# Performance work log

Measured on AMD Instinct MI355X. Metric: run time of the kernel, lower is better.

Reference implementation:

```python
import jax, jax.numpy as jnp
import numpy as np

B, S, D = 8, 1024, 1024
N_HEAD, N_ACTIVE, D_ATTN = 16, 4, 128

def setup_inputs() -> dict:
    key = jax.random.key(0)
    ks = jax.random.split(key, 8)
    sc = 0.02
    return {
        "x": jax.random.normal(ks[0], (B, S, D), jnp.float32),
        "Wq": jax.random.normal(ks[1], (N_HEAD, D, D_ATTN), jnp.float32) * sc,
        "bq": jnp.zeros((N_HEAD, D_ATTN), jnp.float32),
        "Wk": jax.random.normal(ks[2], (N_HEAD, D, D_ATTN), jnp.float32) * sc,
        "bk": jnp.zeros((N_HEAD, D_ATTN), jnp.float32),
        "Wv": jax.random.normal(ks[3], (N_HEAD, D, D_ATTN), jnp.float32) * sc,
        "bv": jnp.zeros((N_HEAD, D_ATTN), jnp.float32),
        "Wr": jax.random.normal(ks[4], (D, N_HEAD), jnp.float32) * sc,
        "br": jnp.zeros((N_HEAD,), jnp.float32),
        "Wo": jax.random.normal(ks[5], (N_ACTIVE * D_ATTN, D), jnp.float32) * sc,
        "bo": jnp.zeros((D,), jnp.float32),
    }

def reference(x, Wq, bq, Wk, bk, Wv, bv, Wr, br, Wo, bo):
    # ---- routing: mean-pool router logits over seq, softmax over heads ----
    logits = jnp.einsum('bsd,dh->bsh', x, Wr) + br          # [B,S,H]
    dist = jax.nn.softmax(logits.mean(axis=1), axis=-1)     # [B,H]
    vals, idx = jax.lax.top_k(dist, N_ACTIVE)               # [B,A]
    # zeros + scatter of top-k probs, then softmax over ALL heads (as in source)
    sparse = jnp.zeros_like(dist).at[jnp.arange(B)[:, None], idx].set(vals)
    gates_full = jax.nn.softmax(sparse, axis=-1)            # [B,H]
    gates = jnp.take_along_axis(gates_full, idx, axis=-1)   # [B,A]
    # ---- gather active-head projection weights per batch ----
    Wq_a, Wk_a, Wv_a = Wq[idx], Wk[idx], Wv[idx]            # [B,A,D,Dk]
    bq_a, bk_a, bv_a = bq[idx], bk[idx], bv[idx]            # [B,A,Dk]
    Q = jnp.einsum('bsd,badk->bask', x, Wq_a) + bq_a[:, :, None, :]
    K = jnp.einsum('bsd,badk->bask', x, Wk_a) + bk_a[:, :, None, :]
    V = jnp.einsum('bsd,badk->bask', x, Wv_a) + bv_a[:, :, None, :]
    scale = 1.0 / jnp.sqrt(jnp.asarray(D_ATTN, x.dtype))
    scores = jax.nn.softmax(jnp.einsum('bask,batk->bast', Q, K) * scale, axis=-1)
    heads = jnp.einsum('bast,batk->bask', scores, V)        # [B,A,S,Dk]
    heads = heads * gates[:, :, None, None]                 # gate each head
    # concat active heads -> [B,S,A*Dk], output projection
    cat = heads.transpose(0, 2, 1, 3).reshape(B, S, N_ACTIVE * D_ATTN)
    return jnp.einsum('bsf,fd->bsd', cat, Wo) + bo
```

## Files before the change

### kernel.cpp

```cpp
#include <hip/hip_runtime.h>
#include <math.h>

#define NB 8
#define SQ 1024
#define DM 1024
#define NH 16
#define NA 4
#define DKH 128

#define WS_XPART 0
#define WS_IDX   524288
#define WS_GATES 524416
#define WS_XB    524800
#define WS_WQT   (WS_XB  + 16777216)
#define WS_WKT   (WS_WQT + 4194304)
#define WS_WVT   (WS_WKT + 4194304)
#define WS_WOT   (WS_WVT + 4194304)
#define WS_Q     (WS_WOT + 1048576)
#define WS_K     (WS_Q  + 8388608)
#define WS_VT    (WS_K  + 8388608)
#define WS_CAT   (WS_VT + 8388608)

typedef __attribute__((ext_vector_type(8))) short short8;
typedef __attribute__((ext_vector_type(4))) short short4v;
typedef __attribute__((ext_vector_type(4))) float f32x4;

#define MFMA16(a, b, c) __builtin_amdgcn_mfma_f32_16x16x32_bf16(a, b, c, 0, 0, 0)
#define GLL16(g, l) __builtin_amdgcn_global_load_lds( \
    (const __attribute__((address_space(1))) void*)(g), \
    (__attribute__((address_space(3))) void*)(l), 16, 0, 0)

__device__ __forceinline__ short f2bf(float f) {
  unsigned u = __float_as_uint(f);
  u += 0x7FFF + ((u >> 16) & 1);
  return (short)(u >> 16);
}

__global__ __launch_bounds__(256) void k_prep(const float* __restrict__ x,
                                              short* __restrict__ xb,
                                              float* __restrict__ xpart) {
  int b = blockIdx.x, ch = blockIdx.y;
  const float* xp = x + ((size_t)b*SQ + (size_t)ch*64)*DM;
  short* xbp = xb + ((size_t)b*SQ + (size_t)ch*64)*DM;
  int t = threadIdx.x;
  float a0 = 0.f, a1 = 0.f, a2 = 0.f, a3 = 0.f;
  #pragma unroll 4
  for (int r = 0; r < 64; r++) {
    float4 v = *(const float4*)&xp[(size_t)r*DM + t*4];
    short4v s4;
    s4[0] = f2bf(v.x); s4[1] = f2bf(v.y); s4[2] = f2bf(v.z); s4[3] = f2bf(v.w);
    *(short4v*)&xbp[(size_t)r*DM + t*4] = s4;
    a0 += v.x; a1 += v.y; a2 += v.z; a3 += v.w;
  }
  float4 o = {a0, a1, a2, a3};
  *(float4*)&xpart[((size_t)b*16 + ch)*DM + t*4] = o;
}

__global__ __launch_bounds__(256) void k_tc(const float* __restrict__ in,
                                            short* __restrict__ outb, int R, int C) {
  __shared__ float t[32][33];
  int bz = blockIdx.z;
  in   += (size_t)bz * R * C;
  outb += (size_t)bz * R * C;
  int r0 = blockIdx.x * 32, c0 = blockIdx.y * 32;
  int tx = threadIdx.x, ty = threadIdx.y;
  #pragma unroll
  for (int i = 0; i < 4; i++)
    t[ty + 8*i][tx] = in[(size_t)(r0 + ty + 8*i) * C + c0 + tx];
  __syncthreads();
  #pragma unroll
  for (int i = 0; i < 4; i++)
    outb[(size_t)(c0 + ty + 8*i) * R + r0 + tx] = f2bf(t[tx][ty + 8*i]);
}

__global__ __launch_bounds__(256) void k_tcqkv(
    const float* __restrict__ Wq, const float* __restrict__ Wk,
    const float* __restrict__ Wv, short* __restrict__ Wqt,
    short* __restrict__ Wkt, short* __restrict__ Wvt) {
  __shared__ float t[32][33];
  int z = blockIdx.z;
  int m = z >> 4, hh = z & 15;
  const float* in = (m == 0 ? Wq : m == 1 ? Wk : Wv) + (size_t)hh * DM * DKH;
  short* outb = (m == 0 ? Wqt : m == 1 ? Wkt : Wvt) + (size_t)hh * DM * DKH;
  int r0 = blockIdx.x * 32, c0 = blockIdx.y * 32;
  int tx = threadIdx.x, ty = threadIdx.y;
  #pragma unroll
  for (int i = 0; i < 4; i++)
    t[ty + 8*i][tx] = in[(size_t)(r0 + ty + 8*i) * DKH + c0 + tx];
  __syncthreads();
  #pragma unroll
  for (int i = 0; i < 4; i++)
    outb[(size_t)(c0 + ty + 8*i) * DM + r0 + tx] = f2bf(t[tx][ty + 8*i]);
}

__global__ __launch_bounds__(256) void k_router(const float* __restrict__ xpart,
                                                const float* __restrict__ Wr,
                                                const float* __restrict__ br,
                                                int* __restrict__ idxout,
                                                float* __restrict__ gatesout) {
  __shared__ float xm[DM];
  __shared__ float red[16][17];
  __shared__ float logits[NH];
  int b = blockIdx.x;
  int t = threadIdx.x;
  #pragma unroll
  for (int i = 0; i < 4; i++) {
    int d = t + 256*i;
    float s = 0.f;
    for (int c = 0; c < 16; c++) s += xpart[((size_t)b*16 + c)*DM + d];
    xm[d] = s * (1.0f/(float)SQ);
  }
  __syncthreads();
  {
    int h = t & 15, c16 = t >> 4;
    float p = 0.f;
    #pragma unroll 8
    for (int j = 0; j < 64; j++) {
      int d = c16*64 + j;
      p += xm[d] * Wr[(size_t)d*NH + h];
    }
    red[c16][h] = p;
  }
  __syncthreads();
  if (t < NH) {
    float lg = br[t];
    #pragma unroll
    for (int c = 0; c < 16; c++) lg += red[c][t];
    logits[t] = lg;
  }
  __syncthreads();
  if (t == 0) {
    float mx = logits[0];
    for (int h = 1; h < NH; h++) mx = fmaxf(mx, logits[h]);
    float e[NH], sum = 0.f;
    for (int h = 0; h < NH; h++) { e[h] = expf(logits[h]-mx); sum += e[h]; }
    float dist[NH];
    for (int h = 0; h < NH; h++) dist[h] = e[h]/sum;
    int idx[NA]; float vals[NA]; bool used[NH];
    for (int h = 0; h < NH; h++) used[h] = false;
    for (int a = 0; a < NA; a++) {
      int best = -1; float bv = -1.f;
      for (int h = 0; h < NH; h++)
        if (!used[h] && dist[h] > bv) { bv = dist[h]; best = h; }
      used[best] = true; idx[a] = best; vals[a] = bv;
    }
    float sp[NH];
    for (int h = 0; h < NH; h++) sp[h] = 0.f;
    for (int a = 0; a < NA; a++) sp[idx[a]] = vals[a];
    float m2 = sp[0];
    for (int h = 1; h < NH; h++) m2 = fmaxf(m2, sp[h]);
    float e2[NH], s2 = 0.f;
    for (int h = 0; h < NH; h++) { e2[h] = expf(sp[h]-m2); s2 += e2[h]; }
    for (int a = 0; a < NA; a++) {
      idxout[b*NA + a]   = idx[a];
      gatesout[b*NA + a] = e2[idx[a]] / s2;
    }
  }
}

__global__ __launch_bounds__(256) void k_qkv(
    const short* __restrict__ xb, const short* __restrict__ Wqt,
    const short* __restrict__ Wkt, const short* __restrict__ Wvt,
    const float* __restrict__ bq, const float* __restrict__ bk,
    const float* __restrict__ bv, const int* __restrict__ idxb,
    short* __restrict__ Qo, short* __restrict__ Ko, short* __restrict__ Vto) {
  __shared__ __align__(16) short As[2][128*64];
  __shared__ __align__(16) short Bs[2][128*64];
  int mt = blockIdx.x, which = blockIdx.y, z = blockIdx.z;
  int b = z >> 2;
  int h = idxb[z];
  const short* Wt; const float* bias;
  if (which == 0)      { Wt = Wqt; bias = bq; }
  else if (which == 1) { Wt = Wkt; bias = bk; }
  else                 { Wt = Wvt; bias = bv; }
  Wt += (size_t)h * (DKH * DM);
  bias += h * DKH;
  const short* Ag = xb + (size_t)b*SQ*DM + (size_t)mt*128*DM;
  int tid = threadIdx.x, lane = tid & 63, wid = tid >> 6;
  int wm = wid & 1, wn = wid >> 1;
  int l15 = lane & 15, quad = lane >> 4, l7 = lane & 7, lby8 = lane >> 3;
  int srow = lby8;
  int scol = ((l7 ^ lby8) * 8);
  f32x4 acc[4][4];
  #pragma unroll
  for (int i = 0; i < 4; i++)
    #pragma unroll
    for (int j = 0; j < 4; j++) acc[i][j] = (f32x4){0.f,0.f,0.f,0.f};
  #pragma unroll
  for (int i = 0; i < 4; i++) {
    int ci = wid*4 + i;
    GLL16(Ag + (size_t)(ci*8 + srow)*DM + scol, &As[0][ci*512]);
    GLL16(Wt + (size_t)(ci*8 + srow)*DM + scol, &Bs[0][ci*512]);
  }
  for (int kt = 0; kt < 16; kt++) {
    int cur = kt & 1;
    asm volatile("s_waitcnt vmcnt(0)" ::: "memory");
    __syncthreads();
    if (kt + 1 < 16) {
      #pragma unroll
      for (int i = 0; i < 4; i++) {
        int ci = wid*4 + i;
        GLL16(Ag + (size_t)(ci*8 + srow)*DM + (kt+1)*64 + scol, &As[cur^1][ci*512]);
        GLL16(Wt + (size_t)(ci*8 + srow)*DM + (kt+1)*64 + scol, &Bs[cur^1][ci*512]);
      }
    }
    #pragma unroll
    for (int ks = 0; ks < 2; ks++) {
      int kc = ks*4 + quad;
      short8 a[4], bf[4];
      #pragma unroll
      for (int mi = 0; mi < 4; mi++)
        a[mi] = *(const short8*)&As[cur][(wm*64 + mi*16 + l15)*64 + ((kc ^ l7)*8)];
      #pragma unroll
      for (int ni = 0; ni < 4; ni++)
        bf[ni] = *(const short8*)&Bs[cur][(wn*64 + ni*16 + l15)*64 + ((kc ^ l7)*8)];
      #pragma unroll
      for (int mi = 0; mi < 4; mi++)
        #pragma unroll
        for (int ni = 0; ni < 4; ni++)
          acc[mi][ni] = MFMA16(a[mi], bf[ni], acc[mi][ni]);
    }
  }
  if (which < 2) {
    short* outp = (which == 0 ? Qo : Ko) + (size_t)z*SQ*DKH;
    #pragma unroll
    for (int mi = 0; mi < 4; mi++)
      #pragma unroll
      for (int ni = 0; ni < 4; ni++) {
        int col = wn*64 + ni*16 + l15;
        float bcol = bias[col];
        #pragma unroll
        for (int r = 0; r < 4; r++) {
          int row = mt*128 + wm*64 + mi*16 + quad*4 + r;
          outp[(size_t)row*DKH + col] = f2bf(acc[mi][ni][r] + bcol);
        }
      }
  } else {
    short* outp = Vto + (size_t)z*DKH*SQ;
    #pragma unroll
    for (int mi = 0; mi < 4; mi++)
      #pragma unroll
      for (int ni = 0; ni < 4; ni++) {
        int col = wn*64 + ni*16 + l15;
        float bcol = bias[col];
        int row0 = mt*128 + wm*64 + mi*16 + quad*4;
        short4v v;
        #pragma unroll
        for (int r = 0; r < 4; r++) v[r] = f2bf(acc[mi][ni][r] + bcol);
        *(short4v*)&outp[(size_t)col*SQ + row0] = v;
      }
  }
}

__global__ __launch_bounds__(256) void k_attn(
    const short* __restrict__ Qg, const short* __restrict__ Kg,
    const short* __restrict__ Vtg, const float* __restrict__ gates,
    short* __restrict__ cat) {
  __shared__ __align__(16) short Ks[2][64*128];
  __shared__ __align__(16) short Vts[2][128*64];
  __shared__ __align__(16) short Ps[4*16*72];
  int qt = blockIdx.x, z = blockIdx.y, b = z >> 2, hs = z & 3;
  int tid = threadIdx.x, lane = tid & 63, wid = tid >> 6;
  int l15 = lane & 15, quad = lane >> 4, l7 = lane & 7, lby8 = lane >> 3;
  const short* Qp = Qg + ((size_t)z*SQ + (size_t)qt*64)*DKH;
  const short* Kp = Kg + (size_t)z*SQ*DKH;
  const short* Vp = Vtg + (size_t)z*DKH*SQ;
  short8 qa[4];
  #pragma unroll
  for (int ks = 0; ks < 4; ks++)
    qa[ks] = *(const short8*)&Qp[(size_t)(wid*16 + l15)*DKH + (ks*4 + quad)*8];
  #pragma unroll
  for (int i = 0; i < 4; i++) {
    int ci = wid*4 + i;
    int r = ci*4 + quad;
    int sc = ((l15 ^ (r & 15)) * 8);
    GLL16(Kp + (size_t)r*DKH + sc, &Ks[0][ci*512]);
    int rv = ci*8 + lby8;
    int scv = ((l7 ^ lby8) * 8);
    GLL16(Vp + (size_t)rv*SQ + scv, &Vts[0][ci*512]);
  }
  f32x4 O[8];
  #pragma unroll
  for (int dn = 0; dn < 8; dn++) O[dn] = (f32x4){0.f,0.f,0.f,0.f};
  float lsum[4] = {0.f, 0.f, 0.f, 0.f};
  const float scale = 0.08838834764831845f;
  for (int t = 0; t < 16; t++) {
    int cur = t & 1;
    asm volatile("s_waitcnt vmcnt(0)" ::: "memory");
    __syncthreads();
    if (t + 1 < 16) {
      #pragma unroll
      for (int i = 0; i < 4; i++) {
        int ci = wid*4 + i;
        int r = ci*4 + quad;
        int sc = ((l15 ^ (r & 15)) * 8);
        GLL16(Kp + (size_t)((t+1)*64 + r)*DKH + sc, &Ks[cur^1][ci*512]);
        int rv = ci*8 + lby8;
        int scv = ((l7 ^ lby8) * 8);
        GLL16(Vp + (size_t)rv*SQ + (t+1)*64 + scv, &Vts[cur^1][ci*512]);
      }
    }
    f32x4 s[4];
    #pragma unroll
    for (int nj = 0; nj < 4; nj++) s[nj] = (f32x4){0.f,0.f,0.f,0.f};
    #pragma unroll
    for (int ks = 0; ks < 4; ks++) {
      int kc = ks*4 + quad;
      #pragma unroll
      for (int nj = 0; nj < 4; nj++) {
        short8 bk8 = *(const short8*)&Ks[cur][(nj*16 + l15)*128 + ((kc ^ l15)*8)];
        s[nj] = MFMA16(qa[ks], bk8, s[nj]);
      }
    }
    #pragma unroll
    for (int r = 0; r < 4; r++) {
      float p0 = __expf(s[0][r]*scale);
      float p1 = __expf(s[1][r]*scale);
      float p2 = __expf(s[2][r]*scale);
      float p3 = __expf(s[3][r]*scale);
      lsum[r] += p0 + p1 + p2 + p3;
      int pbase = wid*1152 + (quad*4 + r)*72;
      Ps[pbase +  0 + l15] = f2bf(p0);
      Ps[pbase + 16 + l15] = f2bf(p1);
      Ps[pbase + 32 + l15] = f2bf(p2);
      Ps[pbase + 48 + l15] = f2bf(p3);
    }
    asm volatile("s_waitcnt lgkmcnt(0)" ::: "memory");
    #pragma unroll
    for (int ks2 = 0; ks2 < 2; ks2++) {
      int kc = ks2*4 + quad;
      short8 pa = *(const short8*)&Ps[wid*1152 + l15*72 + kc*8];
      #pragma unroll
      for (int dn = 0; dn < 8; dn++) {
        short8 bv8 = *(const short8*)&Vts[cur][(dn*16 + l15)*64 + ((kc ^ l7)*8)];
        O[dn] = MFMA16(pa, bv8, O[dn]);
      }
    }
  }
  float gate = gates[z];
  #pragma unroll
  for (int r = 0; r < 4; r++) {
    float rs = lsum[r];
    rs += __shfl_xor(rs, 1); rs += __shfl_xor(rs, 2);
    rs += __shfl_xor(rs, 4); rs += __shfl_xor(rs, 8);
    float sc2 = gate / rs;
    int row = qt*64 + wid*16 + quad*4 + r;
    short* cp = cat + ((size_t)(b*SQ + row))*(NA*DKH) + hs*DKH;
    #pragma unroll
    for (int dn = 0; dn < 8; dn++)
      cp[dn*16 + l15] = f2bf(O[dn][r] * sc2);
  }
}

__global__ __launch_bounds__(256) void k_out(
    const short* __restrict__ catb, const short* __restrict__ Wot,
    const float* __restrict__ bo, float* __restrict__ out) {
  __shared__ __align__(16) short As[2][128*64];
  __shared__ __align__(16) short Bs[2][128*64];
  int mt = blockIdx.x, nt = blockIdx.y;
  const short* Ag = catb + (size_t)mt*128*(NA*DKH);
  const short* Bg = Wot + (size_t)nt*128*(NA*DKH);
  int tid = threadIdx.x, lane = tid & 63, wid = tid >> 6;
  int wm = wid & 1, wn = wid >> 1;
  int l15 = lane & 15, quad = lane >> 4, l7 = lane & 7, lby8 = lane >> 3;
  int srow = lby8;
  int scol = ((l7 ^ lby8) * 8);
  f32x4 acc[4][4];
  #pragma unroll
  for (int i = 0; i < 4; i++)
    #pragma unroll
    for (int j = 0; j < 4; j++) acc[i][j] = (f32x4){0.f,0.f,0.f,0.f};
  #pragma unroll
  for (int i = 0; i < 4; i++) {
    int ci = wid*4 + i;
    GLL16(Ag + (size_t)(ci*8 + srow)*(NA*DKH) + scol, &As[0][ci*512]);
    GLL16(Bg + (size_t)(ci*8 + srow)*(NA*DKH) + scol, &Bs[0][ci*512]);
  }
  for (int kt = 0; kt < 8; kt++) {
    int cur = kt & 1;
    asm volatile("s_waitcnt vmcnt(0)" ::: "memory");
    __syncthreads();
    if (kt + 1 < 8) {
      #pragma unroll
      for (int i = 0; i < 4; i++) {
        int ci = wid*4 + i;
        GLL16(Ag + (size_t)(ci*8 + srow)*(NA*DKH) + (kt+1)*64 + scol, &As[cur^1][ci*512]);
        GLL16(Bg + (size_t)(ci*8 + srow)*(NA*DKH) + (kt+1)*64 + scol, &Bs[cur^1][ci*512]);
      }
    }
    #pragma unroll
    for (int ks = 0; ks < 2; ks++) {
      int kc = ks*4 + quad;
      short8 a[4], bf[4];
      #pragma unroll
      for (int mi = 0; mi < 4; mi++)
        a[mi] = *(const short8*)&As[cur][(wm*64 + mi*16 + l15)*64 + ((kc ^ l7)*8)];
      #pragma unroll
      for (int ni = 0; ni < 4; ni++)
        bf[ni] = *(const short8*)&Bs[cur][(wn*64 + ni*16 + l15)*64 + ((kc ^ l7)*8)];
      #pragma unroll
      for (int mi = 0; mi < 4; mi++)
        #pragma unroll
        for (int ni = 0; ni < 4; ni++)
          acc[mi][ni] = MFMA16(a[mi], bf[ni], acc[mi][ni]);
    }
  }
  #pragma unroll
  for (int mi = 0; mi < 4; mi++)
    #pragma unroll
    for (int ni = 0; ni < 4; ni++) {
      int col = nt*128 + wn*64 + ni*16 + l15;
      float bcol = bo[col];
      #pragma unroll
      for (int r = 0; r < 4; r++) {
        int row = mt*128 + wm*64 + mi*16 + quad*4 + r;
        out[(size_t)row*DM + col] = acc[mi][ni][r] + bcol;
      }
    }
}

extern "C" void kernel_launch(void* const* d_in, const int* in_sizes, int n_in,
                              void* d_out, int out_size, void* d_ws, size_t ws_size,
                              hipStream_t stream) {
  const float* x  = (const float*)d_in[0];
  const float* Wq = (const float*)d_in[1];
  const float* bq = (const float*)d_in[2];
  const float* Wk = (const float*)d_in[3];
  const float* bk = (const float*)d_in[4];
  const float* Wv = (const float*)d_in[5];
  const float* bv = (const float*)d_in[6];
  const float* Wr = (const float*)d_in[7];
  const float* br = (const float*)d_in[8];
  const float* Wo = (const float*)d_in[9];
  const float* bo = (const float*)d_in[10];
  char* ws = (char*)d_ws;
  float* xpart = (float*)(ws + WS_XPART);
  int*   idxb  = (int*)(ws + WS_IDX);
  float* gat   = (float*)(ws + WS_GATES);
  short* xb    = (short*)(ws + WS_XB);
  short* Wqt   = (short*)(ws + WS_WQT);
  short* Wkt   = (short*)(ws + WS_WKT);
  short* Wvt   = (short*)(ws + WS_WVT);
  short* Wot   = (short*)(ws + WS_WOT);
  short* Qb    = (short*)(ws + WS_Q);
  short* Kb    = (short*)(ws + WS_K);
  short* Vtb   = (short*)(ws + WS_VT);
  short* catb  = (short*)(ws + WS_CAT);
  float* out   = (float*)d_out;

  k_prep<<<dim3(NB,16), 256, 0, stream>>>(x, xb, xpart);
  k_router<<<NB, 256, 0, stream>>>(xpart, Wr, br, idxb, gat);
  k_tcqkv<<<dim3(32,4,48), dim3(32,8), 0, stream>>>(Wq, Wk, Wv, Wqt, Wkt, Wvt);
  k_tc<<<dim3(16,32,1), dim3(32,8), 0, stream>>>(Wo, Wot, NA*DKH, DM);
  k_qkv<<<dim3(8,3,NB*NA), 256, 0, stream>>>(xb, Wqt, Wkt, Wvt, bq, bk, bv, idxb, Qb, Kb, Vtb);
  k_attn<<<dim3(16,NB*NA), 256, 0, stream>>>(Qb, Kb, Vtb, gat, catb);
  k_out<<<dim3(64,8), 256, 0, stream>>>(catb, Wot, bo, out);
}
```

Baseline: 237.5 us.

## Fuse weight transposes, flatten grids with XCD-aware block mapping, single-buffer QKV GEMM

Merges the Wq/Wk/Wv and Wo transpose kernels into one launch, which saves a kernel launch. The QKV, attention and output kernels now use 1D grids whose block-index mapping spreads work across the MI355X chiplets (XCDs), so blocks that share inputs land in the same L2. The QKV GEMM drops LDS double buffering and loads each tile synchronously between two barriers. That halves LDS use and should raise occupancy, but global-load latency is no longer overlapped with MFMA work.

Result: faster. 227.6 us (-4.1%).

```diff
diff --git a/kernel.cpp b/kernel.cpp
--- a/kernel.cpp
+++ b/kernel.cpp
@@ -56,13 +56,10 @@
   *(float4*)&xpart[((size_t)b*16 + ch)*DM + t*4] = o;
 }
 
-__global__ __launch_bounds__(256) void k_tc(const float* __restrict__ in,
-                                            short* __restrict__ outb, int R, int C) {
-  __shared__ float t[32][33];
-  int bz = blockIdx.z;
-  in   += (size_t)bz * R * C;
-  outb += (size_t)bz * R * C;
-  int r0 = blockIdx.x * 32, c0 = blockIdx.y * 32;
+__device__ __forceinline__ void tc_tile(const float* __restrict__ in,
+                                        short* __restrict__ outb,
+                                        int R, int C, int r0, int c0,
+                                        float (*t)[33]) {
   int tx = threadIdx.x, ty = threadIdx.y;
   #pragma unroll
   for (int i = 0; i < 4; i++)
@@ -73,24 +70,28 @@
     outb[(size_t)(c0 + ty + 8*i) * R + r0 + tx] = f2bf(t[tx][ty + 8*i]);
 }
 
-__global__ __launch_bounds__(256) void k_tcqkv(
+__global__ __launch_bounds__(256) void k_tw(
     const float* __restrict__ Wq, const float* __restrict__ Wk,
-    const float* __restrict__ Wv, short* __restrict__ Wqt,
-    short* __restrict__ Wkt, short* __restrict__ Wvt) {
+    const float* __restrict__ Wv, const float* __restrict__ Wo,
+    short* __restrict__ Wqt, short* __restrict__ Wkt,
+    short* __restrict__ Wvt, short* __restrict__ Wot) {
   __shared__ float t[32][33];
-  int z = blockIdx.z;
-  int m = z >> 4, hh = z & 15;
-  const float* in = (m == 0 ? Wq : m == 1 ? Wk : Wv) + (size_t)hh * DM * DKH;
-  short* outb = (m == 0 ? Wqt : m == 1 ? Wkt : Wvt) + (size_t)hh * DM * DKH;
-  int r0 = blockIdx.x * 32, c0 = blockIdx.y * 32;
-  int tx = threadIdx.x, ty = threadIdx.y;
-  #pragma unroll
-  for (int i = 0; i < 4; i++)
-    t[ty + 8*i][tx] = in[(size_t)(r0 + ty + 8*i) * DKH + c0 + tx];
-  __syncthreads();
-  #pragma unroll
-  for (int i = 0; i < 4; i++)
-    outb[(size_t)(c0 + ty + 8*i) * DM + r0 + tx] = f2bf(t[tx][ty + 8*i]);
+  int blk = blockIdx.x;
+  if (blk < 6144) {
+    int zz = blk >> 7;
+    int within = blk & 127;
+    int m = zz >> 4, hh = zz & 15;
+    const float* in = (m == 0 ? Wq : m == 1 ? Wk : Wv) + (size_t)hh * DM * DKH;
+    short* outb = (m == 0 ? Wqt : m == 1 ? Wkt : Wvt) + (size_t)hh * DM * DKH;
+    int r0 = (within & 31) * 32;
+    int c0 = (within >> 5) * 32;
+    tc_tile(in, outb, DM, DKH, r0, c0, t);
+  } else {
+    int w2 = blk - 6144;
+    int r0 = (w2 & 15) * 32;
+    int c0 = (w2 >> 4) * 32;
+    tc_tile(Wo, Wot, NA*DKH, DM, r0, c0, t);
+  }
 }
 
 __global__ __launch_bounds__(256) void k_router(const float* __restrict__ xpart,
@@ -164,10 +165,16 @@
     const float* __restrict__ bq, const float* __restrict__ bk,
     const float* __restrict__ bv, const int* __restrict__ idxb,
     short* __restrict__ Qo, short* __restrict__ Ko, short* __restrict__ Vto) {
-  __shared__ __align__(16) short As[2][128*64];
-  __shared__ __align__(16) short Bs[2][128*64];
-  int mt = blockIdx.x, which = blockIdx.y, z = blockIdx.z;
-  int b = z >> 2;
+  __shared__ __align__(16) short As[128*64];
+  __shared__ __align__(16) short Bs[128*64];
+  int blk = blockIdx.x;
+  int b = blk & 7;
+  int rest = blk >> 3;
+  int a4 = rest & 3;
+  int rem = rest >> 2;
+  int which = rem % 3;
+  int mt = rem / 3;
+  int z = b*NA + a4;
   int h = idxb[z];
   const short* Wt; const float* bias;
   if (which == 0)      { Wt = Wqt; bias = bq; }
@@ -186,34 +193,25 @@
   for (int i = 0; i < 4; i++)
     #pragma unroll
     for (int j = 0; j < 4; j++) acc[i][j] = (f32x4){0.f,0.f,0.f,0.f};
-  #pragma unroll
-  for (int i = 0; i < 4; i++) {
-    int ci = wid*4 + i;
-    GLL16(Ag + (size_t)(ci*8 + srow)*DM + scol, &As[0][ci*512]);
-    GLL16(Wt + (size_t)(ci*8 + srow)*DM + scol, &Bs[0][ci*512]);
-  }
   for (int kt = 0; kt < 16; kt++) {
-    int cur = kt & 1;
-    asm volatile("s_waitcnt vmcnt(0)" ::: "memory");
     __syncthreads();
-    if (kt + 1 < 16) {
-      #pragma unroll
-      for (int i = 0; i < 4; i++) {
-        int ci = wid*4 + i;
-        GLL16(Ag + (size_t)(ci*8 + srow)*DM + (kt+1)*64 + scol, &As[cur^1][ci*512]);
-        GLL16(Wt + (size_t)(ci*8 + srow)*DM + (kt+1)*64 + scol, &Bs[cur^1][ci*512]);
-      }
-    }
+    #pragma unroll
+    for (int i = 0; i < 4; i++) {
+      int ci = wid*4 + i;
+      GLL16(Ag + (size_t)(ci*8 + srow)*DM + kt*64 + scol, &As[ci*512]);
+      GLL16(Wt + (size_t)(ci*8 + srow)*DM + kt*64 + scol, &Bs[ci*512]);
+    }
+    __syncthreads();
     #pragma unroll
     for (int ks = 0; ks < 2; ks++) {
       int kc = ks*4 + quad;
       short8 a[4], bf[4];
       #pragma unroll
       for (int mi = 0; mi < 4; mi++)
-        a[mi] = *(const short8*)&As[cur][(wm*64 + mi*16 + l15)*64 + ((kc ^ l7)*8)];
+        a[mi] = *(const short8*)&As[(wm*64 + mi*16 + l15)*64 + ((kc ^ l7)*8)];
       #pragma unroll
       for (int ni = 0; ni < 4; ni++)
-        bf[ni] = *(const short8*)&Bs[cur][(wn*64 + ni*16 + l15)*64 + ((kc ^ l7)*8)];
+        bf[ni] = *(const short8*)&Bs[(wn*64 + ni*16 + l15)*64 + ((kc ^ l7)*8)];
       #pragma unroll
       for (int mi = 0; mi < 4; mi++)
         #pragma unroll
@@ -259,7 +257,11 @@
   __shared__ __align__(16) short Ks[2][64*128];
   __shared__ __align__(16) short Vts[2][128*64];
   __shared__ __align__(16) short Ps[4*16*72];
-  int qt = blockIdx.x, z = blockIdx.y, b = z >> 2, hs = z & 3;
+  int blk = blockIdx.x;
+  int slot = blk >> 3;
+  int z = (blk & 7) + 8*(slot & 3);
+  int qt = slot >> 2;
+  int b = z >> 2, hs = z & 3;
   int tid = threadIdx.x, lane = tid & 63, wid = tid >> 6;
   int l15 = lane & 15, quad = lane >> 4, l7 = lane & 7, lby8 = lane >> 3;
   const short* Qp = Qg + ((size_t)z*SQ + (size_t)qt*64)*DKH;
@@ -357,7 +359,9 @@
     const float* __restrict__ bo, float* __restrict__ out) {
   __shared__ __align__(16) short As[2][128*64];
   __shared__ __align__(16) short Bs[2][128*64];
-  int mt = blockIdx.x, nt = blockIdx.y;
+  int blk = blockIdx.x;
+  int mt = (blk & 7) + 8*(blk >> 6);
+  int nt = (blk >> 3) & 7;
   const short* Ag = catb + (size_t)mt*128*(NA*DKH);
   const short* Bg = Wot + (size_t)nt*128*(NA*DKH);
   int tid = threadIdx.x, lane = tid & 63, wid = tid >> 6;
@@ -450,9 +454,8 @@
 
   k_prep<<<dim3(NB,16), 256, 0, stream>>>(x, xb, xpart);
   k_router<<<NB, 256, 0, stream>>>(xpart, Wr, br, idxb, gat);
-  k_tcqkv<<<dim3(32,4,48), dim3(32,8), 0, stream>>>(Wq, Wk, Wv, Wqt, Wkt, Wvt);
-  k_tc<<<dim3(16,32,1), dim3(32,8), 0, stream>>>(Wo, Wot, NA*DKH, DM);
-  k_qkv<<<dim3(8,3,NB*NA), 256, 0, stream>>>(xb, Wqt, Wkt, Wvt, bq, bk, bv, idxb, Qb, Kb, Vtb);
-  k_attn<<<dim3(16,NB*NA), 256, 0, stream>>>(Qb, Kb, Vtb, gat, catb);
-  k_out<<<dim3(64,8), 256, 0, stream>>>(catb, Wot, bo, out);
-}
+  k_tw<<<6656, dim3(32,8), 0, stream>>>(Wq, Wk, Wv, Wo, Wqt, Wkt, Wvt, Wot);
+  k_qkv<<<768, 256, 0, stream>>>(xb, Wqt, Wkt, Wvt, bq, bk, bv, idxb, Qb, Kb, Vtb);
+  k_attn<<<512, 256, 0, stream>>>(Qb, Kb, Vtb, gat, catb);
+  k_out<<<512, 256, 0, stream>>>(catb, Wot, bo, out);
+}
```
